# Performance work log

Hardware: AMD Instinct MI355X
Metric: run time of the kernel (lower is better)

The kernel has to match this reference:

```python
import jax, jax.numpy as jnp
import numpy as np

B, M, D = 16, 2048, 768
H = 12
Hd = D // H      # 64
HALF = Hd // 2   # 32
SCALE = Hd ** -0.5


def _rotate_half(x):
    # interleaved pair rotation: (x0,x1,x2,x3,...) -> (-x1,x0,-x3,x2,...)
    xe = x[..., ::2]
    xo = x[..., 1::2]
    return jnp.stack((-xo, xe), axis=-1).reshape(x.shape)


def _apply_rope2d(q, k, cos_y, sin_y, cos_x, sin_x):
    # q, k: [B, H, M, Hd]; caches: [M, HALF] -> broadcast as [1,1,M,HALF]
    cy = cos_y[None, None]
    sy = sin_y[None, None]
    cx = cos_x[None, None]
    sx = sin_x[None, None]
    qy, qx = q[..., :HALF], q[..., HALF:]
    ky, kx = k[..., :HALF], k[..., HALF:]
    qy = qy * cy + _rotate_half(qy) * sy
    qx = qx * cx + _rotate_half(qx) * sx
    ky = ky * cy + _rotate_half(ky) * sy
    kx = kx * cx + _rotate_half(kx) * sx
    return jnp.concatenate([qy, qx], axis=-1), jnp.concatenate([ky, kx], axis=-1)


def setup_inputs() -> dict:
    key = jax.random.key(0)
    ks = jax.random.split(key, 14)
    w_std = 0.02
    inp = {
        "x": jax.random.normal(ks[0], (B, M, D), dtype=jnp.float32),
        "cos_y": jax.random.uniform(ks[1], (M, HALF), dtype=jnp.float32),
        "sin_y": jax.random.uniform(ks[2], (M, HALF), dtype=jnp.float32),
        "cos_x": jax.random.uniform(ks[3], (M, HALF), dtype=jnp.float32),
        "sin_x": jax.random.uniform(ks[4], (M, HALF), dtype=jnp.float32),
        "Wq": jax.random.normal(ks[5], (D, D), dtype=jnp.float32) * w_std,
        "bq": jnp.zeros((D,), dtype=jnp.float32),
        "Wk": jax.random.normal(ks[6], (D, D), dtype=jnp.float32) * w_std,
        "bk": jnp.zeros((D,), dtype=jnp.float32),
        "Wv": jax.random.normal(ks[7], (D, D), dtype=jnp.float32) * w_std,
        "bv": jnp.zeros((D,), dtype=jnp.float32),
        "Wo": jax.random.normal(ks[8], (D, D), dtype=jnp.float32) * w_std,
        "bo": jnp.zeros((D,), dtype=jnp.float32),
    }
    return inp


def reference(x, cos_y, sin_y, cos_x, sin_x, Wq, bq, Wk, bk, Wv, bv, Wo, bo):
    # projections: [B, M, D] -> [B, H, M, Hd]
    def proj(W, b):
        return (x @ W + b).reshape(B, M, H, Hd).transpose(0, 2, 1, 3)

    q = proj(Wq, bq)
    k = proj(Wk, bk)
    v = proj(Wv, bv)
    q, k = _apply_rope2d(q, k, cos_y, sin_y, cos_x, sin_x)
    # scaled dot product attention (no mask, no dropout at inference)
    scores = jnp.einsum("bhqd,bhkd->bhqk", q, k) * SCALE
    attn = jax.nn.softmax(scores, axis=-1)
    out = jnp.einsum("bhqk,bhkd->bhqd", attn, v)
    out = out.transpose(0, 2, 1, 3).reshape(B, M, D)
    return out @ Wo + bo
```

## Files before the change

### kernel.cpp

```cpp
#include <hip/hip_runtime.h>
#include <hip/hip_bf16.h>
#include <stdint.h>

typedef __attribute__((ext_vector_type(4))) float f32x4;
typedef __attribute__((ext_vector_type(8))) short s16x8;
typedef __attribute__((ext_vector_type(4))) unsigned short u16x4;
typedef unsigned short u16;

#define NB 16
#define NM 2048
#define ND 768
#define NH 12
#define NROWS (NB*NM)
#define QSCALE 0.18033688011112042f

__device__ __forceinline__ u16 bf16rn(float v) {
  union { float f; uint32_t u; } x; x.f = v;
  uint32_t r = x.u + 0x7FFFu + ((x.u >> 16) & 1u);
  return (u16)(r >> 16);
}
__device__ __forceinline__ uint32_t f2u(float f) {
  union { float f; uint32_t u; } x; x.f = f; return x.u;
}

__device__ __forceinline__ f32x4 mfma16(s16x8 a, s16x8 b, f32x4 c) {
  return __builtin_amdgcn_mfma_f32_16x16x32_bf16(a, b, c, 0, 0, 0);
}

#define GLOAD16(g, s) __builtin_amdgcn_global_load_lds( \
    (__attribute__((address_space(1))) void*)(g), \
    (__attribute__((address_space(3))) void*)(s), 16, 0, 0)

__global__ void k_splitx_hi(const float* __restrict__ x, u16* __restrict__ xh) {
  const int n4 = NROWS * ND / 4;
  for (int i = blockIdx.x * blockDim.x + threadIdx.x; i < n4;
       i += gridDim.x * blockDim.x) {
    f32x4 v = ((const f32x4*)x)[i];
    u16x4 hv;
#pragma unroll
    for (int j = 0; j < 4; ++j) hv[j] = bf16rn(v[j]);
    ((u16x4*)xh)[i] = hv;
  }
}

__global__ void k_prep_w(const float* __restrict__ Wq, const float* __restrict__ Wk,
                         const float* __restrict__ Wv, const float* __restrict__ Wo,
                         u16* __restrict__ wth) {
  int idx = blockIdx.x * 256 + threadIdx.x;
  if (idx >= 3072 * 768) return;
  int j = idx / 768, k = idx % 768;
  int mat = j / 768;
  int jj = j - mat * 768;
  const float* W = (mat == 0) ? Wq : (mat == 1) ? Wk : (mat == 2) ? Wv : Wo;
  wth[idx] = bf16rn(W[k * 768 + jj]);
}

__global__ __launch_bounds__(256, 3) void k_qkv(
    const u16* __restrict__ xh, const u16* __restrict__ wth,
    const float* __restrict__ bq, const float* __restrict__ bk,
    const float* __restrict__ bv,
    const float* __restrict__ cy, const float* __restrict__ sy,
    const float* __restrict__ cx, const float* __restrict__ sx,
    u16* __restrict__ Qh, u16* __restrict__ Kh, u16* __restrict__ Vth)
{
  __shared__ char lds[32768];
  const int t = threadIdx.x, l = t & 63, w = t >> 6;
  const int lr = l & 15, lg = l >> 4;
  const int bid = blockIdx.x;
  const int swz = (bid & 7) * 576 + (bid >> 3);
  const int n0 = (swz / 18) * 128;
  const int j0 = (swz % 18) * 128;
  const int wr = w >> 1, wc = w & 1;
  f32x4 acc[4][4] = {};

  for (int kt = 0; kt < 12; ++kt) {
    const int k0 = kt * 64;
    __syncthreads();
#pragma unroll
    for (int i = 0; i < 4; ++i) {
      int o = (i * 4 + w) * 1024 + l * 16;
      int r = o >> 7;
      int gb = (o & 127) ^ ((r & 7) << 4);
      size_t ga = ((size_t)(n0 + r) * 768 + k0) * 2 + gb;
      size_t gw = ((size_t)(j0 + r) * 768 + k0) * 2 + gb;
      GLOAD16((const char*)xh + ga, lds + o);
      GLOAD16((const char*)wth + gw, lds + 16384 + o);
    }
    __syncthreads();
#pragma unroll
    for (int s = 0; s < 2; ++s) {
      s16x8 ah[4], bh_[4];
#pragma unroll
      for (int mi = 0; mi < 4; ++mi) {
        int r = wr * 64 + mi * 16 + lr;
        int off = r * 128 + ((s * 64 + lg * 16) ^ ((r & 7) << 4));
        ah[mi] = *(const s16x8*)(lds + off);
      }
#pragma unroll
      for (int ni = 0; ni < 4; ++ni) {
        int r = wc * 64 + ni * 16 + lr;
        int off = r * 128 + ((s * 64 + lg * 16) ^ ((r & 7) << 4));
        bh_[ni] = *(const s16x8*)(lds + 16384 + off);
      }
#pragma unroll
      for (int mi = 0; mi < 4; ++mi)
#pragma unroll
        for (int ni = 0; ni < 4; ++ni)
          acc[mi][ni] = mfma16(ah[mi], bh_[ni], acc[mi][ni]);
    }
  }

#pragma unroll
  for (int ni = 0; ni < 4; ++ni) {
    const int col = j0 + wc * 64 + ni * 16 + lr;
    const int mat = col / 768;
    const int cj = col % 768;
    const int h = cj >> 6, d = cj & 63;
    const float bias = (mat == 0 ? bq : mat == 1 ? bk : bv)[cj];
    const float* ct = (d < 32) ? cy : cx;
    const float* st = (d < 32) ? sy : sx;
    const int e = d & 31;
    const bool odd = (d & 1) != 0;
#pragma unroll
    for (int mi = 0; mi < 4; ++mi) {
      const int nbase = n0 + wr * 64 + mi * 16 + lg * 4;
      if (mat == 2) {
        const int b = nbase >> 11, m = nbase & 2047;
        const size_t off = ((size_t)(b * 12 + h) * 64 + d) * 2048 + m;
        u16x4 hv;
#pragma unroll
        for (int r = 0; r < 4; ++r) hv[r] = bf16rn(acc[mi][ni][r] + bias);
        *(u16x4*)(Vth + off) = hv;
      } else {
#pragma unroll
        for (int r = 0; r < 4; ++r) {
          const int n = nbase + r;
          const int b = n >> 11, m = n & 2047;
          float v = acc[mi][ni][r] + bias;
          float p = __shfl_xor(v, 1);
          float c = ct[m * 32 + e], sn = st[m * 32 + e];
          float ov = odd ? (v * c + p * sn) : (v * c - p * sn);
          if (mat == 0) ov *= QSCALE;
          const size_t off = ((size_t)(b * 12 + h) * 2048 + m) * 64 + d;
          (mat == 0 ? Qh : Kh)[off] = bf16rn(ov);
        }
      }
    }
  }
}

__global__ __launch_bounds__(256, 3) void k_attn(
    const u16* __restrict__ Qh, const u16* __restrict__ Kh,
    const u16* __restrict__ Vth, u16* __restrict__ Oh)
{
  __shared__ char lds[49152];
  const int t = threadIdx.x, l = t & 63, w = t >> 6;
  const int lr = l & 15, lg = l >> 4;
  const int bid = blockIdx.x;
  const int swz = (bid & 7) * 384 + (bid >> 3);
  const int bh = swz >> 4;
  const int q0 = (swz & 15) * 128;
  const size_t base = (size_t)bh * (2048 * 64);

  s16x8 qf[2][2];
#pragma unroll
  for (int mi = 0; mi < 2; ++mi)
#pragma unroll
    for (int ks = 0; ks < 2; ++ks) {
      size_t off = base + (size_t)(q0 + w * 32 + mi * 16 + lr) * 64 + ks * 32 + lg * 8;
      qf[mi][ks] = *(const s16x8*)(Qh + off);
    }

  f32x4 oacc[2][4] = {};
  float lsum[2] = {0.f, 0.f};

  char* pP = lds + 32768 + w * 4096;

  auto STAGE = [&](int b, int kc) {
    const int km0 = kc * 64;
#pragma unroll
    for (int i = 0; i < 2; ++i) {
      int o = (i * 4 + w) * 1024 + l * 16;
      int r = o >> 7;
      int gb = (o & 127) ^ ((r & 7) << 4);
      size_t gk = (base + (size_t)(km0 + r) * 64) * 2 + gb;
      size_t gv = (base + (size_t)r * 2048 + km0) * 2 + gb;
      GLOAD16((const char*)Kh + gk, lds + b * 16384 + o);
      GLOAD16((const char*)Vth + gv, lds + b * 16384 + 8192 + o);
    }
  };

  STAGE(0, 0);
  asm volatile("s_waitcnt vmcnt(0)" ::: "memory");
  __syncthreads();

  for (int kc = 0; kc < 32; ++kc) {
    const int cur = kc & 1;
    if (kc < 31) STAGE(cur ^ 1, kc + 1);
    const char* kv = lds + cur * 16384;

    f32x4 s[4][2] = {};
#pragma unroll
    for (int ks = 0; ks < 2; ++ks) {
      s16x8 kb[4];
#pragma unroll
      for (int ni = 0; ni < 4; ++ni) {
        int r = ni * 16 + lr;
        int off = r * 128 + ((ks * 64 + lg * 16) ^ ((r & 7) << 4));
        kb[ni] = *(const s16x8*)(kv + off);
      }
#pragma unroll
      for (int ni = 0; ni < 4; ++ni)
#pragma unroll
        for (int mi = 0; mi < 2; ++mi)
          s[ni][mi] = mfma16(kb[ni], qf[mi][ks], s[ni][mi]);
    }

#pragma unroll
    for (int mi = 0; mi < 2; ++mi) {
      const int row = mi * 16 + lr;
      const int rb = row * 128, sw = (row & 7) << 4;
      float rs = 0.f;
#pragma unroll
      for (int ni = 0; ni < 4; ++ni) {
        float p0 = __builtin_amdgcn_exp2f(s[ni][mi][0]);
        float p1 = __builtin_amdgcn_exp2f(s[ni][mi][1]);
        float p2 = __builtin_amdgcn_exp2f(s[ni][mi][2]);
        float p3 = __builtin_amdgcn_exp2f(s[ni][mi][3]);
        rs += (p0 + p1) + (p2 + p3);
        uint32_t a = __byte_perm(f2u(p0), f2u(p1), 0x7632);
        uint32_t b = __byte_perm(f2u(p2), f2u(p3), 0x7632);
        *(uint2*)(pP + rb + ((32 * ni + 8 * lg) ^ sw)) = make_uint2(a, b);
      }
      lsum[mi] += rs;
    }
    asm volatile("s_waitcnt lgkmcnt(0)" ::: "memory");

#pragma unroll
    for (int ks = 0; ks < 2; ++ks) {
      s16x8 pa[2], vf[4];
#pragma unroll
      for (int mi = 0; mi < 2; ++mi) {
        int row = mi * 16 + lr;
        int off = row * 128 + ((ks * 64 + lg * 16) ^ ((row & 7) << 4));
        pa[mi] = *(const s16x8*)(pP + off);
      }
#pragma unroll
      for (int di = 0; di < 4; ++di) {
        int row = di * 16 + lr;
        int off = row * 128 + ((ks * 64 + lg * 16) ^ ((row & 7) << 4));
        vf[di] = *(const s16x8*)(kv + 8192 + off);
      }
#pragma unroll
      for (int mi = 0; mi < 2; ++mi)
#pragma unroll
        for (int di = 0; di < 4; ++di)
          oacc[mi][di] = mfma16(pa[mi], vf[di], oacc[mi][di]);
    }

    asm volatile("s_waitcnt vmcnt(0)" ::: "memory");
    __syncthreads();
  }

  float ls[2];
#pragma unroll
  for (int mi = 0; mi < 2; ++mi) {
    float v = lsum[mi];
    v += __shfl_xor(v, 16);
    v += __shfl_xor(v, 32);
    ls[mi] = v;
  }

  const int bb = bh / 12, hh = bh % 12;
#pragma unroll
  for (int mi = 0; mi < 2; ++mi)
#pragma unroll
    for (int i = 0; i < 4; ++i) {
      float tot = __shfl(ls[mi], lg * 4 + i);
      float inv = __builtin_amdgcn_rcpf(tot);
      size_t nrow = (size_t)bb * 2048 + q0 + w * 32 + mi * 16 + lg * 4 + i;
#pragma unroll
      for (int di = 0; di < 4; ++di) {
        float v = oacc[mi][di][i] * inv;
        size_t off = nrow * 768 + hh * 64 + di * 16 + lr;
        Oh[off] = bf16rn(v);
      }
    }
}

__global__ __launch_bounds__(256, 3) void k_out(
    const u16* __restrict__ oh, const u16* __restrict__ wth,
    const float* __restrict__ bo, float* __restrict__ out)
{
  __shared__ char lds[32768];
  const int t = threadIdx.x, l = t & 63, w = t >> 6;
  const int lr = l & 15, lg = l >> 4;
  const int bid = blockIdx.x;
  const int swz = (bid & 7) * 192 + (bid >> 3);
  const int n0 = (swz / 6) * 128;
  const int j0 = (swz % 6) * 128;
  const int wr = w >> 1, wc = w & 1;
  f32x4 acc[4][4] = {};

  for (int kt = 0; kt < 12; ++kt) {
    const int k0 = kt * 64;
    __syncthreads();
#pragma unroll
    for (int i = 0; i < 4; ++i) {
      int o = (i * 4 + w) * 1024 + l * 16;
      int r = o >> 7;
      int gb = (o & 127) ^ ((r & 7) << 4);
      size_t ga = ((size_t)(n0 + r) * 768 + k0) * 2 + gb;
      size_t gw = ((size_t)(2304 + j0 + r) * 768 + k0) * 2 + gb;
      GLOAD16((const char*)oh + ga, lds + o);
      GLOAD16((const char*)wth + gw, lds + 16384 + o);
    }
    __syncthreads();
#pragma unroll
    for (int s = 0; s < 2; ++s) {
      s16x8 ah[4], bh_[4];
#pragma unroll
      for (int mi = 0; mi < 4; ++mi) {
        int r = wr * 64 + mi * 16 + lr;
        int off = r * 128 + ((s * 64 + lg * 16) ^ ((r & 7) << 4));
        ah[mi] = *(const s16x8*)(lds + off);
      }
#pragma unroll
      for (int ni = 0; ni < 4; ++ni) {
        int r = wc * 64 + ni * 16 + lr;
        int off = r * 128 + ((s * 64 + lg * 16) ^ ((r & 7) << 4));
        bh_[ni] = *(const s16x8*)(lds + 16384 + off);
      }
#pragma unroll
      for (int mi = 0; mi < 4; ++mi)
#pragma unroll
        for (int ni = 0; ni < 4; ++ni)
          acc[mi][ni] = mfma16(ah[mi], bh_[ni], acc[mi][ni]);
    }
  }
#pragma unroll
  for (int ni = 0; ni < 4; ++ni) {
    const int col = j0 + wc * 64 + ni * 16 + lr;
    const float bias = bo[col];
#pragma unroll
    for (int mi = 0; mi < 4; ++mi) {
      const int nb = n0 + wr * 64 + mi * 16 + lg * 4;
#pragma unroll
      for (int r = 0; r < 4; ++r)
        out[(size_t)(nb + r) * 768 + col] = acc[mi][ni][r] + bias;
    }
  }
}

extern "C" void kernel_launch(void* const* d_in, const int* in_sizes, int n_in,
                              void* d_out, int out_size, void* d_ws, size_t ws_size,
                              hipStream_t stream) {
  const float* x  = (const float*)d_in[0];
  const float* cy = (const float*)d_in[1];
  const float* sy = (const float*)d_in[2];
  const float* cx = (const float*)d_in[3];
  const float* sx = (const float*)d_in[4];
  const float* Wq = (const float*)d_in[5];
  const float* bq = (const float*)d_in[6];
  const float* Wk = (const float*)d_in[7];
  const float* bk = (const float*)d_in[8];
  const float* Wv = (const float*)d_in[9];
  const float* bv = (const float*)d_in[10];
  const float* Wo = (const float*)d_in[11];
  const float* bo = (const float*)d_in[12];
  float* out = (float*)d_out;

  char* ws = (char*)d_ws;
  size_t o = 0;
  const size_t SZ_X = (size_t)NROWS * ND * 2;
  const size_t SZ_W = (size_t)3072 * 768 * 2;
  u16* Xh  = (u16*)(ws + o); o += SZ_X;
  u16* Wth = (u16*)(ws + o); o += SZ_W;
  u16* Vth = (u16*)(ws + o); o += SZ_X;
  u16* Oh  = Xh;

  u16* Qh = (u16*)d_out;
  u16* Kh = Qh + (size_t)NROWS * 768;

  k_splitx_hi<<<2048, 256, 0, stream>>>(x, Xh);
  k_prep_w<<<(3072 * 768 + 255) / 256, 256, 0, stream>>>(Wq, Wk, Wv, Wo, Wth);
  k_qkv<<<4608, 256, 0, stream>>>(Xh, Wth, bq, bk, bv,
                                  cy, sy, cx, sx, Qh, Kh, Vth);
  k_attn<<<3072, 256, 0, stream>>>(Qh, Kh, Vth, Oh);
  k_out<<<1536, 256, 0, stream>>>(Oh, Wth, bo, out);
}
```

Baseline: 472.8 us.

## Build P fragments in registers via permlane swaps instead of LDS round-trip

The attention kernel no longer writes the softmax probabilities P to shared memory and reads them back as MFMA A-operands. Instead it packs them with v_cvt_pk_bf16_f32 and reshuffles lanes with v_permlane32/16_swap so the registers already match the fragment layout for the PV product. This removes the per-wave 4KB LDS scratch and an lgkmcnt wait, which shrinks LDS to 32KB and allows the launch bound to rise to 4 blocks per CU. The cost is extra VALU permute instructions, some register pressure under the tighter launch bound, and correctness depends on the lane mapping being exactly right.

```diff
diff --git a/kernel.cpp b/kernel.cpp
--- a/kernel.cpp
+++ b/kernel.cpp
@@ -149,11 +149,11 @@
   }
 }
 
-__global__ __launch_bounds__(256, 3) void k_attn(
+__global__ __launch_bounds__(256, 4) void k_attn(
     const u16* __restrict__ Qh, const u16* __restrict__ Kh,
     const u16* __restrict__ Vth, u16* __restrict__ Oh)
 {
-  __shared__ char lds[49152];
+  __shared__ char lds[32768];
   const int t = threadIdx.x, l = t & 63, w = t >> 6;
   const int lr = l & 15, lg = l >> 4;
   const int bid = blockIdx.x;
@@ -173,8 +173,7 @@
 
   f32x4 oacc[2][4] = {};
   float lsum[2] = {0.f, 0.f};
-
-  char* pP = lds + 32768 + w * 4096;
+  const f32x4 fz = {0.f, 0.f, 0.f, 0.f};
 
   auto STAGE = [&](int b, int kc) {
     const int km0 = kc * 64;
@@ -199,27 +198,35 @@
     if (kc < 31) STAGE(cur ^ 1, kc + 1);
     const char* kv = lds + cur * 16384;
 
-    f32x4 s[4][2] = {};
-#pragma unroll
-    for (int ks = 0; ks < 2; ++ks) {
+    f32x4 s[4][2];
+    {
       s16x8 kb[4];
 #pragma unroll
       for (int ni = 0; ni < 4; ++ni) {
         int r = ni * 16 + lr;
-        int off = r * 128 + ((ks * 64 + lg * 16) ^ ((r & 7) << 4));
-        kb[ni] = *(const s16x8*)(kv + off);
+        kb[ni] = *(const s16x8*)(kv + r * 128 + ((lg * 16) ^ ((r & 7) << 4)));
       }
 #pragma unroll
       for (int ni = 0; ni < 4; ++ni)
 #pragma unroll
         for (int mi = 0; mi < 2; ++mi)
-          s[ni][mi] = mfma16(kb[ni], qf[mi][ks], s[ni][mi]);
-    }
-
+          s[ni][mi] = mfma16(kb[ni], qf[mi][0], fz);
+#pragma unroll
+      for (int ni = 0; ni < 4; ++ni) {
+        int r = ni * 16 + lr;
+        kb[ni] = *(const s16x8*)(kv + r * 128 + ((64 + lg * 16) ^ ((r & 7) << 4)));
+      }
+#pragma unroll
+      for (int ni = 0; ni < 4; ++ni)
+#pragma unroll
+        for (int mi = 0; mi < 2; ++mi)
+          s[ni][mi] = mfma16(kb[ni], qf[mi][1], s[ni][mi]);
+    }
+
+    s16x8 paf[2][2];
 #pragma unroll
     for (int mi = 0; mi < 2; ++mi) {
-      const int row = mi * 16 + lr;
-      const int rb = row * 128, sw = (row & 7) << 4;
+      uint32_t pk[4][2];
       float rs = 0.f;
 #pragma unroll
       for (int ni = 0; ni < 4; ++ni) {
@@ -228,34 +235,38 @@
         float p2 = __builtin_amdgcn_exp2f(s[ni][mi][2]);
         float p3 = __builtin_amdgcn_exp2f(s[ni][mi][3]);
         rs += (p0 + p1) + (p2 + p3);
-        uint32_t a = __byte_perm(f2u(p0), f2u(p1), 0x7632);
-        uint32_t b = __byte_perm(f2u(p2), f2u(p3), 0x7632);
-        *(uint2*)(pP + rb + ((32 * ni + 8 * lg) ^ sw)) = make_uint2(a, b);
+        asm("v_cvt_pk_bf16_f32 %0, %1, %2" : "=v"(pk[ni][0]) : "v"(p0), "v"(p1));
+        asm("v_cvt_pk_bf16_f32 %0, %1, %2" : "=v"(pk[ni][1]) : "v"(p2), "v"(p3));
       }
       lsum[mi] += rs;
-    }
-    asm volatile("s_waitcnt lgkmcnt(0)" ::: "memory");
-
-#pragma unroll
-    for (int ks = 0; ks < 2; ++ks) {
-      s16x8 pa[2], vf[4];
-#pragma unroll
-      for (int mi = 0; mi < 2; ++mi) {
-        int row = mi * 16 + lr;
-        int off = row * 128 + ((ks * 64 + lg * 16) ^ ((row & 7) << 4));
-        pa[mi] = *(const s16x8*)(pP + off);
-      }
+#pragma unroll
+      for (int c = 0; c < 2; ++c) {
+        uint32_t x0 = pk[2 * c][0], y0 = pk[2 * c + 1][0];
+        uint32_t x1 = pk[2 * c][1], y1 = pk[2 * c + 1][1];
+        asm("v_permlane32_swap_b32 %0, %1" : "+v"(x0), "+v"(y0));
+        asm("v_permlane32_swap_b32 %0, %1" : "+v"(x1), "+v"(y1));
+        asm("v_permlane16_swap_b32 %0, %1" : "+v"(x0), "+v"(y0));
+        asm("v_permlane16_swap_b32 %0, %1" : "+v"(x1), "+v"(y1));
+        union { uint32_t u[4]; s16x8 v; } fr;
+        fr.u[0] = x0; fr.u[1] = x1; fr.u[2] = y0; fr.u[3] = y1;
+        paf[mi][c] = fr.v;
+      }
+    }
+
+#pragma unroll
+    for (int c = 0; c < 2; ++c) {
+      s16x8 vf[4];
 #pragma unroll
       for (int di = 0; di < 4; ++di) {
-        int row = di * 16 + lr;
-        int off = row * 128 + ((ks * 64 + lg * 16) ^ ((row & 7) << 4));
+        int r = di * 16 + lr;
+        int off = r * 128 + ((c * 64 + lg * 16) ^ ((r & 7) << 4));
         vf[di] = *(const s16x8*)(kv + 8192 + off);
       }
 #pragma unroll
       for (int mi = 0; mi < 2; ++mi)
 #pragma unroll
         for (int di = 0; di < 4; ++di)
-          oacc[mi][di] = mfma16(pa[mi], vf[di], oacc[mi][di]);
+          oacc[mi][di] = mfma16(paf[mi][c], vf[di], oacc[mi][di]);
     }
 
     asm volatile("s_waitcnt vmcnt(0)" ::: "memory");
```

After: 457.0 us. -3.3%, faster.
